# Kernel tuning notes

Hardware: AMD Instinct MI355X
Metric: run time of the kernel (lower is better)

Reference implementation:

```python
import jax, jax.numpy as jnp
import numpy as np

N_QUBITS = 4
N_LAYERS = 3
N_FEATURES = 64
BATCH = 524288


def setup_inputs() -> dict:
    key = jax.random.key(0)
    k1, k2, k3, k4 = jax.random.split(key, 4)
    x = jax.random.normal(k1, (BATCH, N_FEATURES), jnp.float32)
    # nn.Linear(64, 4) params
    lim = 1.0 / np.sqrt(N_FEATURES)
    W_pre = jax.random.uniform(k2, (N_QUBITS, N_FEATURES), jnp.float32, -lim, lim)
    b_pre = jax.random.uniform(k3, (N_QUBITS,), jnp.float32, -lim, lim)
    # quantum circuit weights: randn * 0.1
    qweights = jax.random.normal(k4, (N_LAYERS, N_QUBITS, 2), jnp.float32) * 0.1
    return {"x": x, "W_pre": W_pre, "b_pre": b_pre, "qweights": qweights}


def _coef(theta, n):
    # reshape scalar or [B] angle to broadcast against [B, 2,..,2] (n-1 trailing dims after slicing)
    return jnp.reshape(theta, (-1,) + (1,) * (n - 1))


def _apply_ry(state, wire, theta):
    # RY(t) = [[cos t/2, -sin t/2], [sin t/2, cos t/2]] applied on `wire`
    n = state.ndim - 1
    s = jnp.moveaxis(state, 1 + wire, -1)
    a, b = s[..., 0], s[..., 1]
    c = _coef(jnp.cos(theta / 2), n)
    sn = _coef(jnp.sin(theta / 2), n)
    out = jnp.stack([c * a - sn * b, sn * a + c * b], axis=-1)
    return jnp.moveaxis(out, -1, 1 + wire)


def _apply_rz(state, wire, theta):
    # RZ(t) = diag(e^{-i t/2}, e^{+i t/2})
    n = state.ndim - 1
    s = jnp.moveaxis(state, 1 + wire, -1)
    half = _coef(theta / 2, n)
    out = jnp.stack([jnp.exp(-1j * half) * s[..., 0],
                     jnp.exp(1j * half) * s[..., 1]], axis=-1)
    return jnp.moveaxis(out, -1, 1 + wire)


def _apply_cnot(state, ctrl, tgt):
    s = jnp.moveaxis(state, (1 + ctrl, 1 + tgt), (-2, -1))
    s = jnp.concatenate([s[..., 0:1, :], s[..., 1:2, ::-1]], axis=-2)
    return jnp.moveaxis(s, (-2, -1), (1 + ctrl, 1 + tgt))


def _circuit(angles, qweights):
    # batched 4-qubit statevector simulation; state shape [B, 2,2,2,2] (wire 0 = MSB)
    B, n = angles.shape
    nl = qweights.shape[0]
    state = jnp.zeros((B,) + (2,) * n, jnp.complex64)
    state = state.at[(slice(None),) + (0,) * n].set(1.0)
    for w in range(n):
        state = _apply_ry(state, w, angles[:, w])
    for l in range(nl):
        for w in range(n):
            state = _apply_ry(state, w, qweights[l, w, 0])
            state = _apply_rz(state, w, qweights[l, w, 1])
        for w in range(n):
            state = _apply_cnot(state, w, (w + 1) % n)
    probs = state.real ** 2 + state.imag ** 2  # [B, 2,2,2,2] float32
    exps = []
    for w in range(n):
        marg = jnp.moveaxis(probs, 1 + w, 1).reshape(B, 2, -1).sum(-1)  # [B, 2]
        exps.append(marg[:, 0] - marg[:, 1])  # <Z_w>
    return jnp.stack(exps, axis=1)  # [B, n]


def reference(x, W_pre, b_pre, qweights):
    angles = jnp.tanh(x @ W_pre.T + b_pre)  # [B, n_qubits]
    return _circuit(angles, qweights).astype(jnp.float32)
```

## Files before the change

kernel.cpp:

```cpp
#include <hip/hip_runtime.h>
#include <cmath>

__global__ __launch_bounds__(256) void qprep_kernel(
    const float* __restrict__ qw,
    float* __restrict__ A_out)
{
  __shared__ float sre[16][17];
  __shared__ float sim[16][17];
  __shared__ float M[4][16][16];
  const int tid = threadIdx.x;
  const int col = tid >> 4;
  const int u   = tid & 15;

  sre[col][u] = (u == col) ? 1.0f : 0.0f;
  sim[col][u] = 0.0f;
  __syncthreads();

#pragma unroll
  for (int l = 0; l < 3; ++l) {
#pragma unroll
    for (int w = 0; w < 4; ++w) {
      const int mask = 8 >> w;
      float sh, ch, sh2, ch2;
      __sincosf(0.5f * qw[(l * 4 + w) * 2 + 0], &sh, &ch);
      __sincosf(0.5f * qw[(l * 4 + w) * 2 + 1], &sh2, &ch2);
      const int ua = u & ~mask, ub = u | mask;
      const float ar = sre[col][ua], ai = sim[col][ua];
      const float br = sre[col][ub], bi = sim[col][ub];
      __syncthreads();
      float nr, ni;
      if (u & mask) { nr = sh * ar + ch * br; ni = sh * ai + ch * bi; }
      else          { nr = ch * ar - sh * br; ni = ch * ai - sh * bi; }
      float rr, ri;
      if (u & mask) { rr = ch2 * nr - sh2 * ni; ri = ch2 * ni + sh2 * nr; }
      else          { rr = ch2 * nr + sh2 * ni; ri = ch2 * ni - sh2 * nr; }
      sre[col][u] = rr; sim[col][u] = ri;
      __syncthreads();
    }
    int src = u;
    if (src & 1) src ^= 8;
    if (src & 2) src ^= 1;
    if (src & 4) src ^= 2;
    if (src & 8) src ^= 4;
    const float pr = sre[col][src], pi = sim[col][src];
    __syncthreads();
    sre[col][u] = pr; sim[col][u] = pi;
    __syncthreads();
  }

  for (int idx = tid; idx < 1024; idx += 256) {
    const int w = idx >> 8, s = (idx >> 4) & 15, t = idx & 15;
    const int mask = 8 >> w;
    float acc = 0.0f;
#pragma unroll
    for (int uu = 0; uu < 16; ++uu) {
      const float z = (uu & mask) ? -1.0f : 1.0f;
      acc += z * (sre[s][uu] * sre[t][uu] + sim[s][uu] * sim[t][uu]);
    }
    M[w][s][t] = acc;
  }
  __syncthreads();

  for (int idx = tid; idx < 324; idx += 256) {
    const int w = idx & 3, pq = idx >> 2;
    const int p = pq / 9, q = pq % 9;
    const int i0 = p / 3, i1 = p % 3, i2 = q / 3, i3 = q % 3;
    float acc = 0.0f;
#pragma unroll
    for (int comb = 0; comb < 16; ++comb) {
      int s = 0, t = 0;
      float coef = 0.0625f;
      int j;
      j = (comb >> 3) & 1; s |= j << 3; t |= ((i0 == 2) ? (j ^ 1) : j) << 3; if (i0 == 1 && j) coef = -coef;
      j = (comb >> 2) & 1; s |= j << 2; t |= ((i1 == 2) ? (j ^ 1) : j) << 2; if (i1 == 1 && j) coef = -coef;
      j = (comb >> 1) & 1; s |= j << 1; t |= ((i2 == 2) ? (j ^ 1) : j) << 1; if (i2 == 1 && j) coef = -coef;
      j = comb & 1;        s |= j;      t |= ((i3 == 2) ? (j ^ 1) : j);      if (i3 == 1 && j) coef = -coef;
      acc = fmaf(coef, M[w][s][t], acc);
    }
    A_out[idx] = acc;
  }
}

__global__ __launch_bounds__(256) void qmain_kernel(
    const float* __restrict__ x,
    const float* __restrict__ Wp,
    const float* __restrict__ bp,
    const float* __restrict__ A,
    float* __restrict__ out)
{
  __shared__ float xt[256 * 17];
  const int tid = threadIdx.x;
  const size_t row0 = (size_t)blockIdx.x * 256;

  float a0 = 0.f, a1 = 0.f, a2 = 0.f, a3 = 0.f;
#pragma unroll
  for (int c = 0; c < 4; ++c) {
#pragma unroll
    for (int p = 0; p < 4; ++p) {
      const int row = p * 64 + (tid >> 2);
      const int q4 = (tid & 3) << 2;
      const float4 v = *reinterpret_cast<const float4*>(
          x + (row0 + (size_t)row) * 64 + c * 16 + q4);
      float* d = &xt[row * 17 + q4];
      d[0] = v.x; d[1] = v.y; d[2] = v.z; d[3] = v.w;
    }
    __syncthreads();
#pragma unroll
    for (int f = 0; f < 16; ++f) {
      const float xv = xt[tid * 17 + f];
      const int fg = c * 16 + f;
      a0 = fmaf(xv, Wp[fg], a0);
      a1 = fmaf(xv, Wp[64 + fg], a1);
      a2 = fmaf(xv, Wp[128 + fg], a2);
      a3 = fmaf(xv, Wp[192 + fg], a3);
    }
    __syncthreads();
  }

  const float t0 = tanhf(a0 + bp[0]);
  const float t1 = tanhf(a1 + bp[1]);
  const float t2 = tanhf(a2 + bp[2]);
  const float t3 = tanhf(a3 + bp[3]);

  float c0, s0, c1, s1, c2, s2, c3, s3;
  __sincosf(t0, &s0, &c0);
  __sincosf(t1, &s1, &c1);
  __sincosf(t2, &s2, &c2);
  __sincosf(t3, &s3, &c3);

  const float g[9] = {1.f, c1, s1, c0, c0 * c1, c0 * s1, s0, s0 * c1, s0 * s1};
  const float h[9] = {1.f, c3, s3, c2, c2 * c3, c2 * s3, s2, s2 * c3, s2 * s3};

  float e0 = 0.f, e1 = 0.f, e2 = 0.f, e3 = 0.f;
#pragma unroll
  for (int p = 0; p < 9; ++p) {
#pragma unroll
    for (int q = 0; q < 9; ++q) {
      const float t = g[p] * h[q];
      const float* a4 = &A[(p * 9 + q) * 4];
      e0 = fmaf(a4[0], t, e0);
      e1 = fmaf(a4[1], t, e1);
      e2 = fmaf(a4[2], t, e2);
      e3 = fmaf(a4[3], t, e3);
    }
  }
  reinterpret_cast<float4*>(out)[row0 + tid] = make_float4(e0, e1, e2, e3);
}

extern "C" void kernel_launch(void* const* d_in, const int* in_sizes, int n_in,
                              void* d_out, int out_size, void* d_ws, size_t ws_size,
                              hipStream_t stream) {
  const float* x  = (const float*)d_in[0];
  const float* Wp = (const float*)d_in[1];
  const float* bp = (const float*)d_in[2];
  const float* qw = (const float*)d_in[3];
  float* out = (float*)d_out;
  float* A = (float*)d_ws;

  qprep_kernel<<<1, 256, 0, stream>>>(qw, A);

  const int B = in_sizes[0] / 64;
  qmain_kernel<<<B / 256, 256, 0, stream>>>(x, Wp, bp, A, out);
}
```

Baseline: 42.59 us.

## Drop shared-memory transpose; load x rows directly as float4 with fast tanh

The main kernel no longer stages x through an LDS tile with block-wide barriers. Each thread now reads its own 256-byte row straight from global memory as float4 values, software-pipelined against the dot-product FMAs, and reads W and A as float4. tanhf is replaced with an exp/reciprocal approximation, and a waves-per-EU attribute is added to raise occupancy. Per-thread row loads are strided across lanes, so coalescing is worse than in the tiled loads, and the fast tanh gives up a little accuracy.

```diff
diff --git a/kernel.cpp b/kernel.cpp
--- a/kernel.cpp
+++ b/kernel.cpp
@@ -1,5 +1,7 @@
 #include <hip/hip_runtime.h>
+#include <hip/hip_bf16.h>
 #include <cmath>
+
 
 __global__ __launch_bounds__(256) void qprep_kernel(
     const float* __restrict__ qw,
@@ -81,52 +83,65 @@
   }
 }
 
-__global__ __launch_bounds__(256) void qmain_kernel(
+__device__ __forceinline__ float ftanh(float a) {
+  return 1.0f - 2.0f * __builtin_amdgcn_rcpf(__expf(2.0f * a) + 1.0f);
+}
+
+#define DOT(V, I) {                                                         \
+  const float4 w0_ = W4[0 * 16 + (I)];                                      \
+  const float4 w1_ = W4[1 * 16 + (I)];                                      \
+  const float4 w2_ = W4[2 * 16 + (I)];                                      \
+  const float4 w3_ = W4[3 * 16 + (I)];                                      \
+  a0 = fmaf(V.x, w0_.x, a0); a0 = fmaf(V.y, w0_.y, a0);                     \
+  a0 = fmaf(V.z, w0_.z, a0); a0 = fmaf(V.w, w0_.w, a0);                     \
+  a1 = fmaf(V.x, w1_.x, a1); a1 = fmaf(V.y, w1_.y, a1);                     \
+  a1 = fmaf(V.z, w1_.z, a1); a1 = fmaf(V.w, w1_.w, a1);                     \
+  a2 = fmaf(V.x, w2_.x, a2); a2 = fmaf(V.y, w2_.y, a2);                     \
+  a2 = fmaf(V.z, w2_.z, a2); a2 = fmaf(V.w, w2_.w, a2);                     \
+  a3 = fmaf(V.x, w3_.x, a3); a3 = fmaf(V.y, w3_.y, a3);                     \
+  a3 = fmaf(V.z, w3_.z, a3); a3 = fmaf(V.w, w3_.w, a3); }
+
+__global__ __launch_bounds__(256)
+__attribute__((amdgpu_waves_per_eu(8, 8)))
+void qmain_kernel(
     const float* __restrict__ x,
     const float* __restrict__ Wp,
     const float* __restrict__ bp,
-    const float* __restrict__ A,
+    const float4* __restrict__ Aws,
     float* __restrict__ out)
 {
-  __shared__ float xt[256 * 17];
-  const int tid = threadIdx.x;
-  const size_t row0 = (size_t)blockIdx.x * 256;
+  const size_t row = (size_t)blockIdx.x * 256 + threadIdx.x;
+  const float4* xr = reinterpret_cast<const float4*>(x) + row * 16;
+  const float4* W4 = reinterpret_cast<const float4*>(Wp);
 
+  float4 v0 = xr[0], v1 = xr[1], v2 = xr[2], v3 = xr[3];
   float a0 = 0.f, a1 = 0.f, a2 = 0.f, a3 = 0.f;
-#pragma unroll
-  for (int c = 0; c < 4; ++c) {
-#pragma unroll
-    for (int p = 0; p < 4; ++p) {
-      const int row = p * 64 + (tid >> 2);
-      const int q4 = (tid & 3) << 2;
-      const float4 v = *reinterpret_cast<const float4*>(
-          x + (row0 + (size_t)row) * 64 + c * 16 + q4);
-      float* d = &xt[row * 17 + q4];
-      d[0] = v.x; d[1] = v.y; d[2] = v.z; d[3] = v.w;
-    }
-    __syncthreads();
-#pragma unroll
-    for (int f = 0; f < 16; ++f) {
-      const float xv = xt[tid * 17 + f];
-      const int fg = c * 16 + f;
-      a0 = fmaf(xv, Wp[fg], a0);
-      a1 = fmaf(xv, Wp[64 + fg], a1);
-      a2 = fmaf(xv, Wp[128 + fg], a2);
-      a3 = fmaf(xv, Wp[192 + fg], a3);
-    }
-    __syncthreads();
-  }
 
-  const float t0 = tanhf(a0 + bp[0]);
-  const float t1 = tanhf(a1 + bp[1]);
-  const float t2 = tanhf(a2 + bp[2]);
-  const float t3 = tanhf(a3 + bp[3]);
+  DOT(v0, 0);  v0 = xr[4];
+  DOT(v1, 1);  v1 = xr[5];
+  DOT(v2, 2);  v2 = xr[6];
+  DOT(v3, 3);  v3 = xr[7];
+  DOT(v0, 4);  v0 = xr[8];
+  DOT(v1, 5);  v1 = xr[9];
+  DOT(v2, 6);  v2 = xr[10];
+  DOT(v3, 7);  v3 = xr[11];
+  DOT(v0, 8);  v0 = xr[12];
+  DOT(v1, 9);  v1 = xr[13];
+  DOT(v2, 10); v2 = xr[14];
+  DOT(v3, 11); v3 = xr[15];
+  DOT(v0, 12);
+  DOT(v1, 13);
+  DOT(v2, 14);
+  DOT(v3, 15);
+
+  const float t0 = ftanh(a0 + bp[0]);
+  const float t1 = ftanh(a1 + bp[1]);
+  const float t2 = ftanh(a2 + bp[2]);
+  const float t3 = ftanh(a3 + bp[3]);
 
   float c0, s0, c1, s1, c2, s2, c3, s3;
-  __sincosf(t0, &s0, &c0);
-  __sincosf(t1, &s1, &c1);
-  __sincosf(t2, &s2, &c2);
-  __sincosf(t3, &s3, &c3);
+  __sincosf(t0, &s0, &c0); __sincosf(t1, &s1, &c1);
+  __sincosf(t2, &s2, &c2); __sincosf(t3, &s3, &c3);
 
   const float g[9] = {1.f, c1, s1, c0, c0 * c1, c0 * s1, s0, s0 * c1, s0 * s1};
   const float h[9] = {1.f, c3, s3, c2, c2 * c3, c2 * s3, s2, s2 * c3, s2 * s3};
@@ -136,15 +151,13 @@
   for (int p = 0; p < 9; ++p) {
 #pragma unroll
     for (int q = 0; q < 9; ++q) {
-      const float t = g[p] * h[q];
-      const float* a4 = &A[(p * 9 + q) * 4];
-      e0 = fmaf(a4[0], t, e0);
-      e1 = fmaf(a4[1], t, e1);
-      e2 = fmaf(a4[2], t, e2);
-      e3 = fmaf(a4[3], t, e3);
+      const float4 a4 = Aws[p * 9 + q];
+      const float tt = g[p] * h[q];
+      e0 = fmaf(a4.x, tt, e0); e1 = fmaf(a4.y, tt, e1);
+      e2 = fmaf(a4.z, tt, e2); e3 = fmaf(a4.w, tt, e3);
     }
   }
-  reinterpret_cast<float4*>(out)[row0 + tid] = make_float4(e0, e1, e2, e3);
+  reinterpret_cast<float4*>(out)[row] = make_float4(e0, e1, e2, e3);
 }
 
 extern "C" void kernel_launch(void* const* d_in, const int* in_sizes, int n_in,
@@ -156,9 +169,11 @@
   const float* qw = (const float*)d_in[3];
   float* out = (float*)d_out;
   float* A = (float*)d_ws;
+  (void)n_in; (void)out_size; (void)ws_size;
 
   qprep_kernel<<<1, 256, 0, stream>>>(qw, A);
 
   const int B = in_sizes[0] / 64;
-  qmain_kernel<<<B / 256, 256, 0, stream>>>(x, Wp, bp, A, out);
+  qmain_kernel<<<B / 256, 256, 0, stream>>>(x, Wp, bp,
+                                            (const float4*)A, out);
 }
```

Measured after the change: 38.51 us. 1.11x faster.
